# Performance work log

Hardware: AMD Instinct MI355X
Metric: run time of the kernel (lower is better)

The kernel has to match this reference:

```python
import jax, jax.numpy as jnp
import numpy as np

B, N, IN_FT, OUT_FT = 1, 8192, 512, 256


def setup_inputs() -> dict:
    key = jax.random.key(0)
    k1, k2, k3, k4 = jax.random.split(key, 4)
    features = jax.random.normal(k1, (B, N, IN_FT), dtype=jnp.float32)
    adj = jax.random.uniform(k2, (B, N, N), dtype=jnp.float32)
    aug_adj1 = jax.random.uniform(k3, (B, N, N), dtype=jnp.float32)
    # Linear weight (xavier uniform), no bias on the Linear itself
    limit = float(np.sqrt(6.0 / (IN_FT + OUT_FT)))
    W = jax.random.uniform(k4, (OUT_FT, IN_FT), dtype=jnp.float32, minval=-limit, maxval=limit)
    bias = jnp.zeros((OUT_FT,), dtype=jnp.float32)  # GCN bias, filled 0
    prelu_a = jnp.full((1,), 0.25, dtype=jnp.float32)  # PReLU default slope
    return {"features": features, "adj": adj, "aug_adj1": aug_adj1,
            "W": W, "bias": bias, "prelu_a": prelu_a, "sparse": 0}


def _prelu(x, a):
    return jnp.where(x >= 0, x, a * x)


def _gcn(features, adj, W, bias, prelu_a):
    # Linear (no bias): [B,N,in] x [out,in]^T -> [B,N,out]
    seq_fts = jnp.einsum('bni,oi->bno', features, W)
    # Dense adjacency aggregation: bmm(adj, seq_fts)
    out = jnp.einsum('bnm,bmo->bno', adj, seq_fts) + bias
    return _prelu(out, prelu_a)


def reference(features, adj, aug_adj1, W, bias, prelu_a, sparse):
    # sparse flag is static (0 -> dense bmm path)
    h_0 = _gcn(features, adj, W, bias, prelu_a)
    h_1 = _gcn(features, aug_adj1, W, bias, prelu_a)
    return (h_0, h_1)
```

## Files before the change

### kernel.cpp

```cpp
#include <hip/hip_runtime.h>

#define NROW 8192
#define INF  512
#define OUTF 256
#define M_ELEM (NROW * OUTF)
#define NSTEP 32

typedef __bf16 v8bf __attribute__((ext_vector_type(8)));
typedef __bf16 v4bf __attribute__((ext_vector_type(4)));
typedef float  v4f  __attribute__((ext_vector_type(4)));

__device__ __forceinline__ v8bf cvt_bf8(v4f u0, v4f u1) {
  v8bf v;
  v[0]=(__bf16)u0[0]; v[1]=(__bf16)u0[1]; v[2]=(__bf16)u0[2]; v[3]=(__bf16)u0[3];
  v[4]=(__bf16)u1[0]; v[5]=(__bf16)u1[1]; v[6]=(__bf16)u1[2]; v[7]=(__bf16)u1[3];
  return v;
}

__global__ __launch_bounds__(256) void seq_fts_kernel(
    const float* __restrict__ feat, const float* __restrict__ W,
    __bf16* __restrict__ Bp) {
  const int tid  = threadIdx.x;
  const int lane = tid & 63, w = tid >> 6;
  const int llo  = lane & 15, lhi = lane >> 4;
  const int row0 = blockIdx.x * 64;
  const int col0 = w * 64;

  v4f acc[4][4] = {};
#pragma unroll 1
  for (int kb = 0; kb < INF / 32; ++kb) {
    const int kofs = kb * 32 + lhi * 8;
    v8bf a[4], b[4];
#pragma unroll
    for (int i = 0; i < 4; ++i) {
      const float* p = feat + (size_t)(row0 + i * 16 + llo) * INF + kofs;
      a[i] = cvt_bf8(*(const v4f*)p, *(const v4f*)(p + 4));
    }
#pragma unroll
    for (int i = 0; i < 4; ++i) {
      const float* p = W + (size_t)(col0 + i * 16 + llo) * INF + kofs;
      b[i] = cvt_bf8(*(const v4f*)p, *(const v4f*)(p + 4));
    }
#pragma unroll
    for (int ri = 0; ri < 4; ++ri)
#pragma unroll
      for (int ci = 0; ci < 4; ++ci)
        acc[ri][ci] = __builtin_amdgcn_mfma_f32_16x16x32_bf16(
            a[ri], b[ci], acc[ri][ci], 0, 0, 0);
  }
#pragma unroll
  for (int ri = 0; ri < 4; ++ri)
#pragma unroll
    for (int ci = 0; ci < 4; ++ci) {
      const int mf = row0 + ri * 16 + lhi * 4;
      const int o  = col0 + ci * 16 + llo;
      size_t e = (((size_t)(mf >> 5) * 16 + (o >> 4)) * 64 +
                  ((mf >> 3) & 3) * 16 + (o & 15)) * 8 + (mf & 7);
      v4bf v;
      v[0] = (__bf16)acc[ri][ci][0]; v[1] = (__bf16)acc[ri][ci][1];
      v[2] = (__bf16)acc[ri][ci][2]; v[3] = (__bf16)acc[ri][ci][3];
      *(v4bf*)(Bp + e) = v;
    }
}

__global__ __launch_bounds__(512, 1) void gcn_agg_kernel(
    const float* __restrict__ adjA, const float* __restrict__ adjB,
    const __bf16* __restrict__ Bp, const float* __restrict__ bias,
    const float* __restrict__ prelu_a, float* __restrict__ out) {
  const int tid  = threadIdx.x;
  const int lane = tid & 63, w = tid >> 6;
  const int llo  = lane & 15, lhi = lane >> 4;
  const int row0 = blockIdx.x * 64;
  const int z    = blockIdx.y;
  const float* __restrict__ adj = z ? adjB : adjA;

  __shared__ __align__(16) char LdsA[2][65536];

  v4f acc[4][2] = {};

  auto stage_a = [&](int buf, int t) {
#pragma unroll
    for (int i = 0; i < 8; ++i) {
      const int r   = w * 8 + i;
      const int key = ((r & 15) << 1) | ((r >> 3) & 1);
      const float* src =
          adj + (size_t)(row0 + r) * NROW + t * 256 + ((lane ^ key) << 2);
      __builtin_amdgcn_global_load_lds(
          (const __attribute__((address_space(1))) void*)src,
          (__attribute__((address_space(3))) void*)(&LdsA[buf][r * 1024]),
          16, 0, 2 );
    }
  };

  const __bf16* __restrict__ Bpw = Bp + ((size_t)(w * 2) * 64 + lane) * 8;
  auto issue_b = [&](int half, v8bf (&b)[4][2]) {
#pragma unroll
    for (int g = 0; g < 4; ++g)
#pragma unroll
      for (int ci = 0; ci < 2; ++ci)
        b[g][ci] = *(const v8bf*)(
            Bpw + ((size_t)((half * 4 + g) * 16 + ci)) * 512);
  };

  auto compute_half = [&](int buf, int h, v8bf (&b)[4][2]) {
    const char* ab = &LdsA[buf][0];
#pragma unroll
    for (int g = 0; g < 4; ++g) {
      const int kg = h * 4 + g;
      v8bf af[4];
#pragma unroll
      for (int rt = 0; rt < 4; ++rt) {
        const int r   = rt * 16 + llo;
        const int key = ((r & 15) << 1) | ((r >> 3) & 1);
        const char* base = ab + r * 1024;
        v4f u0 = *(const v4f*)(base + (((kg * 8 + lhi * 2    ) ^ key) << 4));
        v4f u1 = *(const v4f*)(base + (((kg * 8 + lhi * 2 + 1) ^ key) << 4));
        af[rt] = cvt_bf8(u0, u1);
      }
#pragma unroll
      for (int ci = 0; ci < 2; ++ci)
#pragma unroll
        for (int rt = 0; rt < 4; ++rt)
          acc[rt][ci] = __builtin_amdgcn_mfma_f32_16x16x32_bf16(
              af[rt], b[g][ci], acc[rt][ci], 0, 0, 0);
    }
  };

  v8bf bX[4][2], bY[4][2];

  stage_a(0, 0);
  issue_b(0, bX);
  __builtin_amdgcn_sched_barrier(0);
  issue_b(1, bY);
  __builtin_amdgcn_sched_barrier(0);
  stage_a(1, 1);
  asm volatile("s_waitcnt vmcnt(24)" ::: "memory");
  __builtin_amdgcn_sched_barrier(0);
  __builtin_amdgcn_s_barrier();

#pragma unroll 1
  for (int t = 0; t < NSTEP; ++t) {
    const int p = t & 1;
    compute_half(p, 0, bX);
    __builtin_amdgcn_sched_barrier(0);
    {
      const int hb = (2 * t + 2 < 2 * NSTEP) ? 2 * t + 2 : 2 * NSTEP - 2;
      issue_b(hb, bX);
    }
    __builtin_amdgcn_sched_barrier(0);
    compute_half(p, 1, bY);
    __builtin_amdgcn_sched_barrier(0);
    {
      const int hb = (2 * t + 3 < 2 * NSTEP) ? 2 * t + 3 : 2 * NSTEP - 1;
      issue_b(hb, bY);
    }
    __builtin_amdgcn_sched_barrier(0);
    __builtin_amdgcn_s_barrier();
    {
      const int ta = (t + 2 < NSTEP) ? t + 2 : NSTEP - 1;
      stage_a(p, ta);
    }
    asm volatile("s_waitcnt vmcnt(24)" ::: "memory");
    __builtin_amdgcn_sched_barrier(0);
    __builtin_amdgcn_s_barrier();
  }
  asm volatile("s_waitcnt vmcnt(0)" ::: "memory");

  const float slope = prelu_a[0];
  float* __restrict__ outp = out + (size_t)z * M_ELEM;
#pragma unroll
  for (int ci = 0; ci < 2; ++ci) {
    const int o  = w * 32 + ci * 16 + llo;
    const float bs = bias[o];
#pragma unroll
    for (int rt = 0; rt < 4; ++rt) {
      const int m = row0 + rt * 16 + lhi * 4;
#pragma unroll
      for (int r = 0; r < 4; ++r) {
        float v = acc[rt][ci][r] + bs;
        outp[(size_t)(m + r) * OUTF + o] = v >= 0.f ? v : slope * v;
      }
    }
  }
}

extern "C" void kernel_launch(void* const* d_in, const int* in_sizes, int n_in,
                              void* d_out, int out_size, void* d_ws, size_t ws_size,
                              hipStream_t stream) {
  const float* feat = (const float*)d_in[0];
  const float* adj  = (const float*)d_in[1];
  const float* aug  = (const float*)d_in[2];
  const float* W    = (const float*)d_in[3];
  const float* bias = (const float*)d_in[4];
  const float* pa   = (const float*)d_in[5];
  float* out = (float*)d_out;
  __bf16* Bp = (__bf16*)d_ws;

  seq_fts_kernel<<<dim3(NROW / 64), 256, 0, stream>>>(feat, W, Bp);
  gcn_agg_kernel<<<dim3(NROW / 64, 2), 512, 0, stream>>>(
      adj, aug, Bp, bias, pa, out);
}
```

Baseline: 169.3 us.

## Split adjacency staging between LDS DMA and register-path nontemporal loads

```diff
diff --git a/kernel.cpp b/kernel.cpp
--- a/kernel.cpp
+++ b/kernel.cpp
@@ -78,9 +78,9 @@
 
   v4f acc[4][2] = {};
 
-  auto stage_a = [&](int buf, int t) {
-#pragma unroll
-    for (int i = 0; i < 8; ++i) {
+  auto stage_a_dma = [&](int buf, int t) {
+#pragma unroll
+    for (int i = 0; i < 4; ++i) {
       const int r   = w * 8 + i;
       const int key = ((r & 15) << 1) | ((r >> 3) & 1);
       const float* src =
@@ -91,6 +91,24 @@
           16, 0, 2 );
     }
   };
+  v4f areg[4];
+  auto issue_a_reg = [&](int t) {
+#pragma unroll
+    for (int i = 0; i < 4; ++i) {
+      const int r = w * 8 + 4 + i;
+      const float* src =
+          adj + (size_t)(row0 + r) * NROW + t * 256 + (lane << 2);
+      areg[i] = __builtin_nontemporal_load((const v4f*)src);
+    }
+  };
+  auto write_a_reg = [&](int buf) {
+#pragma unroll
+    for (int i = 0; i < 4; ++i) {
+      const int r   = w * 8 + 4 + i;
+      const int key = ((r & 15) << 1) | ((r >> 3) & 1);
+      *(v4f*)(&LdsA[buf][r * 1024 + ((lane ^ key) << 4)]) = areg[i];
+    }
+  };
 
   const __bf16* __restrict__ Bpw = Bp + ((size_t)(w * 2) * 64 + lane) * 8;
   auto issue_b = [&](int half, v8bf (&b)[4][2]) {
@@ -128,19 +146,29 @@
 
   v8bf bX[4][2], bY[4][2];
 
-  stage_a(0, 0);
+  stage_a_dma(0, 0);
+  issue_a_reg(0);
+  __builtin_amdgcn_sched_barrier(0);
   issue_b(0, bX);
   __builtin_amdgcn_sched_barrier(0);
   issue_b(1, bY);
   __builtin_amdgcn_sched_barrier(0);
-  stage_a(1, 1);
-  asm volatile("s_waitcnt vmcnt(24)" ::: "memory");
+  stage_a_dma(1, 1);
+  asm volatile("s_waitcnt vmcnt(20)" ::: "memory");
+  __builtin_amdgcn_sched_barrier(0);
+  write_a_reg(0);
+  asm volatile("s_waitcnt lgkmcnt(0)" ::: "memory");
   __builtin_amdgcn_sched_barrier(0);
   __builtin_amdgcn_s_barrier();
 
 #pragma unroll 1
   for (int t = 0; t < NSTEP; ++t) {
     const int p = t & 1;
+    {
+      const int tn = (t + 1 < NSTEP) ? t + 1 : NSTEP - 1;
+      issue_a_reg(tn);
+    }
+    __builtin_amdgcn_sched_barrier(0);
     compute_half(p, 0, bX);
     __builtin_amdgcn_sched_barrier(0);
     {
@@ -158,9 +186,12 @@
     __builtin_amdgcn_s_barrier();
     {
       const int ta = (t + 2 < NSTEP) ? t + 2 : NSTEP - 1;
-      stage_a(p, ta);
-    }
-    asm volatile("s_waitcnt vmcnt(24)" ::: "memory");
+      stage_a_dma(p, ta);
+    }
+    asm volatile("s_waitcnt vmcnt(20)" ::: "memory");
+    __builtin_amdgcn_sched_barrier(0);
+    write_a_reg(p ^ 1);
+    asm volatile("s_waitcnt lgkmcnt(0)" ::: "memory");
     __builtin_amdgcn_sched_barrier(0);
     __builtin_amdgcn_s_barrier();
   }
```

Result: no change. 169.3 us (-0.0%).
